# Kernel tuning notes

Measured on AMD Instinct MI355X. Metric: run time of the kernel, lower is better.

## Reference

```python
import jax, jax.numpy as jnp
import numpy as np

EMBED_DIM = 64
NUM_HEADS = 8
D_K = EMBED_DIM // NUM_HEADS  # 8
B, S = 8, 1024


def setup_inputs() -> dict:
    key = jax.random.key(0)
    ks = jax.random.split(key, 10)
    f32 = jnp.float32
    lim = 1.0 / np.sqrt(EMBED_DIM)
    def lin(k):
        kw, kb = jax.random.split(k)
        w = jax.random.uniform(kw, (EMBED_DIM, EMBED_DIM), f32, -lim, lim)
        b = jax.random.uniform(kb, (EMBED_DIM,), f32, -lim, lim)
        return w, b
    wq, bq = lin(ks[0])
    wk, bk = lin(ks[1])
    wv, bv = lin(ks[2])
    wo, bo = lin(ks[3])
    theta = jax.random.normal(ks[4], (EMBED_DIM,), f32)  # trainable RY angles, one per wire
    x = jax.random.normal(ks[5], (B, S, EMBED_DIM), f32)
    return {"x": x, "wq": wq, "bq": bq, "wk": wk, "bk": bk,
            "wv": wv, "bv": bv, "theta": theta, "wo": wo, "bo": bo}


def _quantum_map(t, theta):
    # Per-qubit circuit on |0>: RX(t_i) encode, RY(theta_i), <PauliZ_i>.
    # Product state => <Z_i> = cos(theta_i) * cos(t_i) exactly.
    return jnp.cos(theta) * jnp.cos(t.reshape(-1, EMBED_DIM))  # [N, E]


def reference(x, wq, bq, wk, bk, wv, bv, theta, wo, bo):
    # Linear QKV (torch nn.Linear: x @ W^T + b)
    q = x @ wq.T + bq
    k = x @ wk.T + bk
    v = x @ wv.T + bv
    # Quantum measurement map, flattened over batch*seq (as in the original)
    q_q = _quantum_map(q, theta)  # [N, E], N = B*S
    k_q = _quantum_map(k, theta)
    v_q = _quantum_map(v, theta)
    # Full flattened attention: [N, N] scores (original never reshapes back)
    scores = (q_q @ k_q.T) / jnp.sqrt(jnp.asarray(D_K, x.dtype))
    attn = jax.nn.softmax(scores, axis=-1)  # dropout is identity in eval
    out = attn @ v_q  # [N, E]
    return out @ wo.T + bo
```

## Files before the change

### kernel.cpp

```cpp
#include <hip/hip_runtime.h>
#include <hip/hip_bf16.h>

#define NQ 8192
#define DIM 64
#define SPLITS 16
#define QBLK 128
#define WQ 64
#define BN 64
#define KEYS_PER_SPLIT (NQ / SPLITS)
#define NTILES (KEYS_PER_SPLIT / BN)
#define GRID_FLASH ((NQ / QBLK) * SPLITS)
#define MERGEB 512
#define MROWS (NQ / MERGEB)
#define SC2 0.51012301920911057f
#define KSTR 72

typedef short s8v __attribute__((ext_vector_type(8)));
typedef short s4v __attribute__((ext_vector_type(4)));
typedef float f4v __attribute__((ext_vector_type(4)));
typedef int   i4v __attribute__((ext_vector_type(4)));

__device__ __forceinline__ float b2f(short s) {
  unsigned int u = ((unsigned int)(unsigned short)s) << 16;
  return __uint_as_float(u);
}
__device__ __forceinline__ short f2b(float f) {
  __hip_bfloat16 h = __float2bfloat16(f);
  return *reinterpret_cast<short*>(&h);
}
__device__ __forceinline__ int pack_bf16x2(float a, float b) {
  union { __hip_bfloat162 h; int i; } u;
  u.h = __float22bfloat162_rn(make_float2(a, b));
  return u.i;
}
__device__ __forceinline__ float fast_exp2(float x) {
#if __has_builtin(__builtin_amdgcn_exp2f)
  return __builtin_amdgcn_exp2f(x);
#else
  return exp2f(x);
#endif
}

__global__ __launch_bounds__(64) void qkv_kernel(
    const float* __restrict__ x,
    const float* __restrict__ wq, const float* __restrict__ bq,
    const float* __restrict__ wk, const float* __restrict__ bk,
    const float* __restrict__ wv, const float* __restrict__ bv,
    const float* __restrict__ theta,
    short* __restrict__ qq, short* __restrict__ kvT) {
  int lane = threadIdx.x & 63;
  int l15 = lane & 15, quad = lane >> 4;
  int tg = blockIdx.x;
  int mg = blockIdx.y;
  int n = tg * 16 + l15;

  const float* W  = (mg == 0) ? wq : (mg == 1) ? wk : wv;
  const float* Bb = (mg == 0) ? bq : (mg == 1) ? bk : bv;

  const float* xr = x + (size_t)n * DIM + quad * 8;
  float4 x0 = *(const float4*)&xr[0];
  float4 x1 = *(const float4*)&xr[4];
  float4 x2 = *(const float4*)&xr[32];
  float4 x3 = *(const float4*)&xr[36];
  s8v xf0 = {f2b(x0.x), f2b(x0.y), f2b(x0.z), f2b(x0.w),
             f2b(x1.x), f2b(x1.y), f2b(x1.z), f2b(x1.w)};
  s8v xf1 = {f2b(x2.x), f2b(x2.y), f2b(x2.z), f2b(x2.w),
             f2b(x3.x), f2b(x3.y), f2b(x3.z), f2b(x3.w)};

  size_t tb = (size_t)(n >> 6) * 8192;
  int nperm = (n & 3) | ((n & 16) >> 2);
  size_t vbase = tb + 4096 + ((n & 32) >> 5) * 2048 + ((n & 15) >> 2) * 128 + nperm;

#pragma unroll
  for (int i = 0; i < 4; ++i) {
    const float* wr = W + (size_t)(i * 16 + l15) * DIM + quad * 8;
    float4 a0 = *(const float4*)&wr[0];
    float4 a1 = *(const float4*)&wr[4];
    float4 a2 = *(const float4*)&wr[32];
    float4 a3 = *(const float4*)&wr[36];
    s8v wf0 = {f2b(a0.x), f2b(a0.y), f2b(a0.z), f2b(a0.w),
               f2b(a1.x), f2b(a1.y), f2b(a1.z), f2b(a1.w)};
    s8v wf1 = {f2b(a2.x), f2b(a2.y), f2b(a2.z), f2b(a2.w),
               f2b(a3.x), f2b(a3.y), f2b(a3.z), f2b(a3.w)};
    f4v acc = (f4v){0.f, 0.f, 0.f, 0.f};
    acc = __builtin_amdgcn_mfma_f32_16x16x32_bf16(wf0, xf0, acc, 0, 0, 0);
    acc = __builtin_amdgcn_mfma_f32_16x16x32_bf16(wf1, xf1, acc, 0, 0, 0);
    int d0 = i * 16 + quad * 4;
    float4 bias = *(const float4*)&Bb[d0];
    float4 th4 = *(const float4*)&theta[d0];
    float y0 = __cosf(acc[0] + bias.x) * __cosf(th4.x);
    float y1 = __cosf(acc[1] + bias.y) * __cosf(th4.y);
    float y2 = __cosf(acc[2] + bias.z) * __cosf(th4.z);
    float y3 = __cosf(acc[3] + bias.w) * __cosf(th4.w);
    if (mg == 0) {
      s4v p = {f2b(SC2 * y0), f2b(SC2 * y1), f2b(SC2 * y2), f2b(SC2 * y3)};
      *(s4v*)&qq[(size_t)n * DIM + d0] = p;
    } else if (mg == 1) {
      int e = d0;
      size_t idx = tb + ((n & 63) >> 4) * 1024 + (e >> 5) * 512 +
                   ((e & 31) >> 3) * 128 + (n & 15) * 8 + (e & 7);
      s4v p = {f2b(y0), f2b(y1), f2b(y2), f2b(y3)};
      *(s4v*)&kvT[idx] = p;
    } else {
      float ys[4] = {y0, y1, y2, y3};
#pragma unroll
      for (int r = 0; r < 4; ++r) {
        int e = d0 + r;
        kvT[vbase + (e >> 4) * 512 + (e & 15) * 8] = f2b(ys[r]);
      }
    }
  }
}

#if __has_builtin(__builtin_amdgcn_global_load_lds)
#define DMA_CHUNK(srcp, dstp) \
  __builtin_amdgcn_global_load_lds( \
      (const __attribute__((address_space(1))) void*)(srcp), \
      (__attribute__((address_space(3))) void*)(dstp), 16, 0, 0)
#else
#define DMA_CHUNK(srcp, dstp) \
  { *(s8v*)((short*)(dstp) + (threadIdx.x & 63) * 8) = \
        *(const s8v*)((const short*)(srcp)); }
#endif

__global__ __launch_bounds__(128, 2) void flash_kernel(
    const short* __restrict__ qq, const short* __restrict__ kvT,
    short* __restrict__ pO, short* __restrict__ pL) {
  __shared__ __align__(16) short lds[2][8192];

  int tid = threadIdx.x;
  int wave = tid >> 6, lane = tid & 63;
  int l15 = lane & 15, quad = lane >> 4;
  int qblock = blockIdx.x >> 4, split = blockIdx.x & 15;
  int qbase = qblock * QBLK + wave * WQ;

  s8v qf[4][2];
#pragma unroll
  for (int qt = 0; qt < 4; ++qt) {
    const short* qr = qq + (qbase + qt * 16 + l15) * DIM + quad * 8;
    qf[qt][0] = *(const s8v*)qr;
    qf[qt][1] = *(const s8v*)(qr + 32);
  }

  const short ONE = (short)0x3F80;
  const s8v ones = {ONE, ONE, ONE, ONE, ONE, ONE, ONE, ONE};

  f4v o[4][4], ol[4];
#pragma unroll
  for (int qt = 0; qt < 4; ++qt) {
    ol[qt] = (f4v){0.f, 0.f, 0.f, 0.f};
#pragma unroll
    for (int c = 0; c < 4; ++c) o[qt][c] = (f4v){0.f, 0.f, 0.f, 0.f};
  }

  int gt0 = split * NTILES;

#define STAGE(T, BUF)                                                        \
  {                                                                          \
    const short* s_ = kvT + (size_t)(gt0 + (T)) * 8192 + wave * 4096 +       \
                      lane * 8;                                              \
    short* d_ = &lds[BUF][wave * 4096];                                      \
    _Pragma("unroll") for (int c2 = 0; c2 < 8; ++c2)                         \
        DMA_CHUNK(s_ + c2 * 512, d_ + c2 * 512);                             \
  }

  STAGE(0, 0)

  for (int t = 0; t < NTILES; ++t) {
    __syncthreads();
    if (t + 1 < NTILES) STAGE(t + 1, (t + 1) & 1)

    const short* kb = lds[t & 1];
    const short* vb = lds[t & 1] + 4096;

#pragma unroll
    for (int kp = 0; kp < 2; ++kp) {
      i4v pai[4];
#pragma unroll
      for (int h = 0; h < 2; ++h) {
        int kt = kp * 2 + h;
        s8v kf0 = *(const s8v*)&kb[(kt * 2) * 512 + lane * 8];
        s8v kf1 = *(const s8v*)&kb[(kt * 2 + 1) * 512 + lane * 8];
#pragma unroll
        for (int qt = 0; qt < 4; ++qt) {
          f4v acc = (f4v){0.f, 0.f, 0.f, 0.f};
          acc = __builtin_amdgcn_mfma_f32_16x16x32_bf16(kf0, qf[qt][0], acc, 0, 0, 0);
          acc = __builtin_amdgcn_mfma_f32_16x16x32_bf16(kf1, qf[qt][1], acc, 0, 0, 0);
          pai[qt][h * 2]     = pack_bf16x2(fast_exp2(acc[0]), fast_exp2(acc[1]));
          pai[qt][h * 2 + 1] = pack_bf16x2(fast_exp2(acc[2]), fast_exp2(acc[3]));
        }
      }
#pragma unroll
      for (int qt = 0; qt < 4; ++qt)
        ol[qt] = __builtin_amdgcn_mfma_f32_16x16x32_bf16(
            __builtin_bit_cast(s8v, pai[qt]), ones, ol[qt], 0, 0, 0);
#pragma unroll
      for (int c = 0; c < 4; ++c) {
        s8v vf = *(const s8v*)&vb[(kp * 4 + c) * 512 + lane * 8];
#pragma unroll
        for (int qt = 0; qt < 4; ++qt)
          o[qt][c] = __builtin_amdgcn_mfma_f32_16x16x32_bf16(
              __builtin_bit_cast(s8v, pai[qt]), vf, o[qt][c], 0, 0, 0);
      }
    }
  }

#pragma unroll
  for (int qt = 0; qt < 4; ++qt) {
#pragma unroll
    for (int r = 0; r < 4; ++r) {
      int q = qbase + qt * 16 + quad * 4 + r;
      short* dst = pO + (size_t)q * (SPLITS * DIM) + split * DIM;
#pragma unroll
      for (int c = 0; c < 4; ++c) dst[c * 16 + l15] = f2b(o[qt][c][r]);
      if (l15 == 0) pL[(size_t)q * SPLITS + split] = f2b(ol[qt][r]);
    }
  }
}

__global__ __launch_bounds__(256) void merge_kernel(
    const short* __restrict__ pO, const short* __restrict__ pL,
    const float* __restrict__ wo, const float* __restrict__ bo,
    float* __restrict__ out) {
  __shared__ __align__(16) short wsh[DIM * KSTR];
  __shared__ __align__(16) float att[MROWS * DIM];
  int tid = threadIdx.x;
  int q0 = blockIdx.x * MROWS;
  for (int i = tid; i < DIM * 16; i += 256) {
    int r = i >> 4, c4 = (i & 15) << 2;
    float4 w = *(const float4*)&wo[r * DIM + c4];
    s4v p = {f2b(w.x), f2b(w.y), f2b(w.z), f2b(w.w)};
    *(s4v*)&wsh[r * KSTR + c4] = p;
  }
  int wave = tid >> 6, j = tid & 63;
#pragma unroll
  for (int i = 0; i < MROWS / 4; ++i) {
    int rr = wave * (MROWS / 4) + i;
    int q = q0 + rr;
    const short* prow = pO + (size_t)q * (SPLITS * DIM);
    s8v v0 = *(const s8v*)&prow[j * 8];
    s8v v1 = *(const s8v*)&prow[512 + j * 8];
    float a[8];
#pragma unroll
    for (int m = 0; m < 8; ++m) a[m] = b2f(v0[m]) + b2f(v1[m]);
#pragma unroll
    for (int st = 8; st < 64; st <<= 1)
#pragma unroll
      for (int m = 0; m < 8; ++m) a[m] += __shfl_xor(a[m], st);
    const short* lrow = pL + (size_t)q * SPLITS;
    s8v lv0 = *(const s8v*)&lrow[0];
    s8v lv1 = *(const s8v*)&lrow[8];
    float l = 0.f;
#pragma unroll
    for (int m = 0; m < 8; ++m) l += b2f(lv0[m]) + b2f(lv1[m]);
#if __has_builtin(__builtin_amdgcn_rcpf)
    float ri = __builtin_amdgcn_rcpf(l);
#else
    float ri = 1.f / l;
#endif
    if (j < 8) {
      float4 f0 = {a[0] * ri, a[1] * ri, a[2] * ri, a[3] * ri};
      float4 f1 = {a[4] * ri, a[5] * ri, a[6] * ri, a[7] * ri};
      *(float4*)&att[rr * DIM + j * 8] = f0;
      *(float4*)&att[rr * DIM + j * 8 + 4] = f1;
    }
  }
  __syncthreads();
  int e = tid & 63, rg = tid >> 6;
  for (int rr = rg; rr < MROWS; rr += 4) {
    float acc = bo[e];
#pragma unroll
    for (int c8 = 0; c8 < 8; ++c8) {
      s8v w = *(const s8v*)&wsh[e * KSTR + c8 * 8];
      const float* ar = &att[rr * DIM + c8 * 8];
      acc += ar[0] * b2f(w[0]) + ar[1] * b2f(w[1]) + ar[2] * b2f(w[2]) + ar[3] * b2f(w[3])
           + ar[4] * b2f(w[4]) + ar[5] * b2f(w[5]) + ar[6] * b2f(w[6]) + ar[7] * b2f(w[7]);
    }
    out[(size_t)(q0 + rr) * DIM + e] = acc;
  }
}

extern "C" void kernel_launch(void* const* d_in, const int* in_sizes, int n_in,
                              void* d_out, int out_size, void* d_ws, size_t ws_size,
                              hipStream_t stream) {
  const float* x  = (const float*)d_in[0];
  const float* wq = (const float*)d_in[1];
  const float* bq = (const float*)d_in[2];
  const float* wk = (const float*)d_in[3];
  const float* bk = (const float*)d_in[4];
  const float* wv = (const float*)d_in[5];
  const float* bv = (const float*)d_in[6];
  const float* th = (const float*)d_in[7];
  const float* wo = (const float*)d_in[8];
  const float* bo = (const float*)d_in[9];

  char* ws = (char*)d_ws;
  short* qq  = (short*)(ws);
  short* kvT = (short*)(ws + (1u << 20));
  short* pO  = (short*)(ws + (3u << 20));
  short* pL  = (short*)(ws + (19u << 20));

  hipLaunchKernelGGL(qkv_kernel, dim3(NQ / 16, 3), dim3(64), 0, stream,
                     x, wq, bq, wk, bk, wv, bv, th, qq, kvT);
  hipLaunchKernelGGL(flash_kernel, dim3(GRID_FLASH), dim3(128), 0, stream,
                     qq, kvT, pO, pL);
  hipLaunchKernelGGL(merge_kernel, dim3(MERGEB), dim3(256), 0, stream,
                     pO, pL, wo, bo, (float*)d_out);
}
```

Baseline: 115.3 us.

## Store split partials split-major and reduce across splits per thread in merge

The flash kernel now writes its partial outputs and row sums in a split-major layout ([split][q][dim]) rather than query-major. The merge kernel is restructured so each thread loops over the 16 splits and accumulates two adjacent bf16 columns, replacing the cross-lane shuffle reduction. The merge grid doubles to 1024 blocks of 8 rows each. s_setprio is also raised around the PV MFMA section to favour matrix-core issue. The aim is to cut the shuffle work in the merge stage and increase its parallelism, at the cost of a more strided write pattern in the flash kernel.

Result: no change. 114.7 us (-0.5%).

```diff
diff --git a/kernel.cpp b/kernel.cpp
--- a/kernel.cpp
+++ b/kernel.cpp
@@ -10,7 +10,7 @@
 #define KEYS_PER_SPLIT (NQ / SPLITS)
 #define NTILES (KEYS_PER_SPLIT / BN)
 #define GRID_FLASH ((NQ / QBLK) * SPLITS)
-#define MERGEB 512
+#define MERGEB 1024
 #define MROWS (NQ / MERGEB)
 #define SC2 0.51012301920911057f
 #define KSTR 72
@@ -23,6 +23,12 @@
 __device__ __forceinline__ float b2f(short s) {
   unsigned int u = ((unsigned int)(unsigned short)s) << 16;
   return __uint_as_float(u);
+}
+__device__ __forceinline__ float b2f_lo(unsigned int u) {
+  return __uint_as_float(u << 16);
+}
+__device__ __forceinline__ float b2f_hi(unsigned int u) {
+  return __uint_as_float(u & 0xffff0000u);
 }
 __device__ __forceinline__ short f2b(float f) {
   __hip_bfloat16 h = __float2bfloat16(f);
@@ -190,6 +196,7 @@
           pai[qt][h * 2 + 1] = pack_bf16x2(fast_exp2(acc[2]), fast_exp2(acc[3]));
         }
       }
+      __builtin_amdgcn_s_setprio(1);
 #pragma unroll
       for (int qt = 0; qt < 4; ++qt)
         ol[qt] = __builtin_amdgcn_mfma_f32_16x16x32_bf16(
@@ -202,6 +209,7 @@
           o[qt][c] = __builtin_amdgcn_mfma_f32_16x16x32_bf16(
               __builtin_bit_cast(s8v, pai[qt]), vf, o[qt][c], 0, 0, 0);
       }
+      __builtin_amdgcn_s_setprio(0);
     }
   }
 
@@ -210,10 +218,10 @@
 #pragma unroll
     for (int r = 0; r < 4; ++r) {
       int q = qbase + qt * 16 + quad * 4 + r;
-      short* dst = pO + (size_t)q * (SPLITS * DIM) + split * DIM;
+      short* dst = pO + ((size_t)split * NQ + q) * DIM;
 #pragma unroll
       for (int c = 0; c < 4; ++c) dst[c * 16 + l15] = f2b(o[qt][c][r]);
-      if (l15 == 0) pL[(size_t)q * SPLITS + split] = f2b(ol[qt][r]);
+      if (l15 == 0) pL[(size_t)split * NQ + q] = f2b(ol[qt][r]);
     }
   }
 }
@@ -232,38 +240,26 @@
     s4v p = {f2b(w.x), f2b(w.y), f2b(w.z), f2b(w.w)};
     *(s4v*)&wsh[r * KSTR + c4] = p;
   }
-  int wave = tid >> 6, j = tid & 63;
-#pragma unroll
-  for (int i = 0; i < MROWS / 4; ++i) {
-    int rr = wave * (MROWS / 4) + i;
-    int q = q0 + rr;
-    const short* prow = pO + (size_t)q * (SPLITS * DIM);
-    s8v v0 = *(const s8v*)&prow[j * 8];
-    s8v v1 = *(const s8v*)&prow[512 + j * 8];
-    float a[8];
-#pragma unroll
-    for (int m = 0; m < 8; ++m) a[m] = b2f(v0[m]) + b2f(v1[m]);
-#pragma unroll
-    for (int st = 8; st < 64; st <<= 1)
-#pragma unroll
-      for (int m = 0; m < 8; ++m) a[m] += __shfl_xor(a[m], st);
-    const short* lrow = pL + (size_t)q * SPLITS;
-    s8v lv0 = *(const s8v*)&lrow[0];
-    s8v lv1 = *(const s8v*)&lrow[8];
-    float l = 0.f;
-#pragma unroll
-    for (int m = 0; m < 8; ++m) l += b2f(lv0[m]) + b2f(lv1[m]);
+  {
+    int e2 = (tid & 31) * 2, rg8 = tid >> 5;
+    int q = q0 + rg8;
+    const short* psrc = pO + (size_t)q * DIM + e2;
+    const short* lsrc = pL + q;
+    float a0 = 0.f, a1 = 0.f, l = 0.f;
+#pragma unroll
+    for (int sp = 0; sp < SPLITS; ++sp) {
+      unsigned int u = *(const unsigned int*)&psrc[(size_t)sp * NQ * DIM];
+      a0 += b2f_lo(u);
+      a1 += b2f_hi(u);
+      l += b2f(lsrc[(size_t)sp * NQ]);
+    }
 #if __has_builtin(__builtin_amdgcn_rcpf)
     float ri = __builtin_amdgcn_rcpf(l);
 #else
     float ri = 1.f / l;
 #endif
-    if (j < 8) {
-      float4 f0 = {a[0] * ri, a[1] * ri, a[2] * ri, a[3] * ri};
-      float4 f1 = {a[4] * ri, a[5] * ri, a[6] * ri, a[7] * ri};
-      *(float4*)&att[rr * DIM + j * 8] = f0;
-      *(float4*)&att[rr * DIM + j * 8 + 4] = f1;
-    }
+    att[rg8 * DIM + e2] = a0 * ri;
+    att[rg8 * DIM + e2 + 1] = a1 * ri;
   }
   __syncthreads();
   int e = tid & 63, rg = tid >> 6;
```
